# Kernel optimization log

Measured on AMD Instinct MI355X. Metric: run time of the kernel, lower is better.

## Reference

```python
import jax, jax.numpy as jnp
import numpy as np

B, C_IN, C_OUT, N, K = 32, 16, 32, 2048, 3


def setup_inputs() -> dict:
    key = jax.random.key(0)
    k1, k2 = jax.random.split(key, 2)
    x = jax.random.normal(k1, (B, C_IN, N), dtype=jnp.float32)
    # Conv1d weight (out_channels, in_channels, K), Kaiming-ish scale
    W = jax.random.normal(k2, (C_OUT, C_IN, K), dtype=jnp.float32) * (1.0 / np.sqrt(C_IN * K))
    b = jnp.zeros((C_OUT,), dtype=jnp.float32)
    return {"x": x, "W": W, "b": b}


def reference(x, W, b):
    # x: (B, C, N) -- tokens are the N column vectors in channel space
    Bd, C, Nd = x.shape
    Kd = W.shape[2]
    # NNT: pairwise squared Euclidean distances between token vectors
    sq = jnp.sum(x * x, axis=1)                      # (B, N)
    gram = jnp.einsum('bcn,bcm->bnm', x, x)          # (B, N, N)
    dist = sq[:, :, None] - 2.0 * gram + sq[:, None, :]  # (B, N, N)
    # K nearest neighbors (smallest distance; self included at dist ~0)
    _, idx = jax.lax.top_k(-dist, Kd)                # (B, N, K) int32
    flat_idx = idx.reshape(Bd, Nd * Kd)              # (B, N*K)
    # gather neighbor columns -> prime: (B, C, N*K)
    prime = jnp.take_along_axis(x, flat_idx[:, None, :], axis=2)
    # Conv1d(kernel=K, stride=K) == per-group contraction over the K neighbors
    prime4 = prime.reshape(Bd, C, Nd, Kd)            # (B, C, N, K)
    out = jnp.einsum('bcnk,ock->bon', prime4, W) + b[None, :, None]
    return out  # (B, C_out, N)
```

## Files before the change

### kernel.cpp

```cpp
#include <hip/hip_runtime.h>
#include <float.h>
#include <limits.h>

#define BATCH 32
#define C_IN 16
#define C_OUT 32
#define NTOK 2048
#define KNN 3
#define ZH 2
#define MSEG (NTOK / ZH)
#define WPB 4

using f32x4v = __attribute__((ext_vector_type(4))) float;
using bf16x8 = __attribute__((ext_vector_type(8))) short;

__device__ __forceinline__ unsigned short f2bf(float f) {
    unsigned u = __float_as_uint(f);
    unsigned r = u + 0x7fffu + ((u >> 16) & 1u);
    return (unsigned short)(r >> 16);
}
__device__ __forceinline__ float bf2f(unsigned short h) {
    return __uint_as_float(((unsigned)h) << 16);
}
__device__ __forceinline__ unsigned umin2(unsigned a, unsigned b) { return a < b ? a : b; }
__device__ __forceinline__ unsigned med3u(unsigned a, unsigned b, unsigned c) {
    unsigned d;
    asm("v_med3_u32 %0, %1, %2, %3" : "=v"(d) : "v"(a), "v"(b), "v"(c));
    return d;
}

__global__ void __launch_bounds__(256) prep_kernel(
    const float* __restrict__ x, float* __restrict__ xTf,
    float* __restrict__ sqf, uint4* __restrict__ Am)
{
    const int n = blockIdx.x * 256 + threadIdx.x;
    const int b = blockIdx.y;
    const float* xb = x + (size_t)b * C_IN * NTOK;

    float v[C_IN];
#pragma unroll
    for (int c = 0; c < C_IN; ++c) v[c] = xb[(size_t)c * NTOK + n];

    float acc = 0.0f;
#pragma unroll
    for (int c = 0; c < C_IN; ++c) acc = __fadd_rn(acc, __fmul_rn(v[c], v[c]));
    sqf[(size_t)b * NTOK + n] = acc;

    float4* dst = (float4*)(xTf + ((size_t)b * NTOK + n) * C_IN);
#pragma unroll
    for (int j = 0; j < 4; ++j)
        dst[j] = make_float4(v[4*j+0], v[4*j+1], v[4*j+2], v[4*j+3]);

    unsigned hw[8], lw[8];
#pragma unroll
    for (int j = 0; j < 8; ++j) {
        const unsigned short h0 = f2bf(v[2*j]),   h1 = f2bf(v[2*j+1]);
        const unsigned short l0 = f2bf(v[2*j]   - bf2f(h0));
        const unsigned short l1 = f2bf(v[2*j+1] - bf2f(h1));
        hw[j] = (unsigned)h0 | ((unsigned)h1 << 16);
        lw[j] = (unsigned)l0 | ((unsigned)l1 << 16);
    }
    uint4* amb = Am + (size_t)b * NTOK * 4;
    const int nt  = n >> 4;
    const int col = n & 15;
    amb[nt*64 + 0*16 + col] = make_uint4(hw[0], hw[1], hw[2], hw[3]);
    amb[nt*64 + 1*16 + col] = make_uint4(hw[4], hw[5], hw[6], hw[7]);
    amb[nt*64 + 2*16 + col] = make_uint4(lw[0], lw[1], lw[2], lw[3]);
    amb[nt*64 + 3*16 + col] = make_uint4(lw[4], lw[5], lw[6], lw[7]);
}

__global__ void __launch_bounds__(256) knn_scan_kernel(
    const uint4* __restrict__ Am, const float* __restrict__ sqf,
    const float* __restrict__ xTf, float* __restrict__ pd, int* __restrict__ pi)
{
    __shared__ int   lds_ci[WPB][16][17];
    __shared__ float lds_de[WPB][16][17];

    const int tid  = threadIdx.x;
    const int w    = tid >> 6;
    const int l    = tid & 63;
    const int col  = l & 15;
    const int quad = l >> 4;

    const int wg   = blockIdx.x;
    const int b_lo = wg & 7;
    const int t2   = wg >> 3;
    const int b_hi = t2 >> 6;
    const int rest = t2 & 63;
    const int z    = rest >> 5;
    const int ntb  = rest & 31;
    const int b    = b_lo + (b_hi << 3);
    const int nt   = ntb * WPB + w;

    const int n  = nt * 16 + col;
    const int mbase = z * MSEG;

    const uint4* amb = Am + (size_t)b * NTOK * 4;
    const float* sqb = sqf + (size_t)b * NTOK;

    const uint4 bh4 = amb[(size_t)nt*64 + ((quad & 1) * 16) + col];
    const uint4 bl4 = amb[(size_t)nt*64 + ((2 + (quad & 1)) * 16) + col];
    const bf16x8 Bhi = *(const bf16x8*)&bh4;
    const bf16x8 Blo = *(const bf16x8*)&bl4;

    const float sqn  = sqb[n];
    const float bias = sqn + 4.0f;

    unsigned k0 = ~0u, k1 = ~0u, k2 = ~0u, k3 = ~0u;
    const int moff = quad * 4;
    const int tgbase = z * (MSEG / 16);

#pragma unroll 2
    for (int t = 0; t < MSEG / 16; ++t) {
        const uint4 af4 = amb[(size_t)(tgbase + t) * 64 + l];
        const bf16x8 Af = *(const bf16x8*)&af4;
        const float4 sq4 = *(const float4*)(sqb + mbase + t * 16 + moff);

        f32x4v acc = {0.0f, 0.0f, 0.0f, 0.0f};
        acc = __builtin_amdgcn_mfma_f32_16x16x32_bf16(Af, Bhi, acc, 0, 0, 0);
        acc = __builtin_amdgcn_mfma_f32_16x16x32_bf16(Af, Blo, acc, 0, 0, 0);

        const int mb = mbase + t * 16 + moff;
        const float sqa[4] = { sq4.x, sq4.y, sq4.z, sq4.w };
#pragma unroll
        for (int r = 0; r < 4; ++r) {
            const float d = __fadd_rn(__fmaf_rn(-2.0f, acc[r], sqa[r]), bias);
            const unsigned key = (__float_as_uint(d) & 0xFFFFF800u) | (unsigned)(mb + r);
            const unsigned ok0 = k0, ok1 = k1, ok2 = k2;
            k0 = umin2(key, k0);
            k1 = med3u(key, ok0, k1);
            k2 = med3u(key, ok1, k2);
            k3 = med3u(key, ok2, k3);
        }
    }

    lds_ci[w][col][quad*4+0] = (int)(k0 & 2047u);
    lds_ci[w][col][quad*4+1] = (int)(k1 & 2047u);
    lds_ci[w][col][quad*4+2] = (int)(k2 & 2047u);
    lds_ci[w][col][quad*4+3] = (int)(k3 & 2047u);
    __syncthreads();

    float xn[C_IN];
    {
        const float4* src = (const float4*)(xTf + ((size_t)b * NTOK + n) * C_IN);
#pragma unroll
        for (int j = 0; j < 4; ++j) {
            const float4 tq = src[j];
            xn[4*j+0] = tq.x; xn[4*j+1] = tq.y; xn[4*j+2] = tq.z; xn[4*j+3] = tq.w;
        }
    }
#pragma unroll
    for (int c = 0; c < 4; ++c) {
        const int cand = quad * 4 + c;
        const int mi = lds_ci[w][col][cand];
        const float4* xm4 = (const float4*)(xTf + ((size_t)b * NTOK + mi) * C_IN);
        const float4 a0 = xm4[0], a1 = xm4[1], a2 = xm4[2], a3 = xm4[3];
        float g = 0.0f;
        g = __fmaf_rn(xn[0],  a0.x, g); g = __fmaf_rn(xn[1],  a0.y, g);
        g = __fmaf_rn(xn[2],  a0.z, g); g = __fmaf_rn(xn[3],  a0.w, g);
        g = __fmaf_rn(xn[4],  a1.x, g); g = __fmaf_rn(xn[5],  a1.y, g);
        g = __fmaf_rn(xn[6],  a1.z, g); g = __fmaf_rn(xn[7],  a1.w, g);
        g = __fmaf_rn(xn[8],  a2.x, g); g = __fmaf_rn(xn[9],  a2.y, g);
        g = __fmaf_rn(xn[10], a2.z, g); g = __fmaf_rn(xn[11], a2.w, g);
        g = __fmaf_rn(xn[12], a3.x, g); g = __fmaf_rn(xn[13], a3.y, g);
        g = __fmaf_rn(xn[14], a3.z, g); g = __fmaf_rn(xn[15], a3.w, g);
        lds_de[w][col][cand] = __fadd_rn(__fmaf_rn(-2.0f, g, sqn), sqb[mi]);
    }
    __syncthreads();

    if (l < 16) {
        float D0 = FLT_MAX, D1 = FLT_MAX, D2 = FLT_MAX;
        int   I0 = INT_MAX, I1 = INT_MAX, I2 = INT_MAX;
#pragma unroll
        for (int c = 0; c < 16; ++c) {
            const float d = lds_de[w][l][c];
            const int  ix = lds_ci[w][l][c];
            const bool b0 = (d < D0) || (d == D0 && ix < I0);
            const bool b1 = (d < D1) || (d == D1 && ix < I1);
            const bool b2 = (d < D2) || (d == D2 && ix < I2);
            const float oD0 = D0, oD1 = D1;
            const int   oI0 = I0, oI1 = I1;
            D0 = b0 ? d : D0;               I0 = b0 ? ix : I0;
            D1 = b0 ? oD0 : (b1 ? d : D1);  I1 = b0 ? oI0 : (b1 ? ix : I1);
            D2 = b1 ? oD1 : (b2 ? d : D2);  I2 = b1 ? oI1 : (b2 ? ix : I2);
        }
        const size_t base = ((size_t)z * KNN * BATCH + b) * NTOK + nt * 16 + l;
        const size_t kstr = (size_t)BATCH * NTOK;
        pd[base + 0*kstr] = D0;  pi[base + 0*kstr] = I0;
        pd[base + 1*kstr] = D1;  pi[base + 1*kstr] = I1;
        pd[base + 2*kstr] = D2;  pi[base + 2*kstr] = I2;
    }
}

__global__ void __launch_bounds__(256) merge_conv_kernel(
    const float* __restrict__ xTf, const float* __restrict__ pd,
    const int* __restrict__ pi, const float* __restrict__ W,
    const float* __restrict__ bias, float* __restrict__ out)
{
    const int wg   = blockIdx.x;
    const int b_lo = wg & 7;
    const int t2   = wg >> 3;
    const int b_hi = t2 >> 3;
    const int xc   = t2 & 7;
    const int b    = b_lo + (b_hi << 3);
    const int n    = xc * 256 + threadIdx.x;

    float D0 = FLT_MAX, D1 = FLT_MAX, D2 = FLT_MAX;
    int   I0 = INT_MAX, I1 = INT_MAX, I2 = INT_MAX;
    const size_t kstr = (size_t)BATCH * NTOK;
#pragma unroll
    for (int z = 0; z < ZH; ++z) {
        const size_t base = ((size_t)z * KNN * BATCH + b) * NTOK + n;
#pragma unroll
        for (int k = 0; k < KNN; ++k) {
            const float d = pd[base + (size_t)k * kstr];
            const int  ix = pi[base + (size_t)k * kstr];
            const bool b0 = (d < D0) || (d == D0 && ix < I0);
            const bool b1 = (d < D1) || (d == D1 && ix < I1);
            const bool b2 = (d < D2) || (d == D2 && ix < I2);
            const float oD0 = D0, oD1 = D1;
            const int   oI0 = I0, oI1 = I1;
            D0 = b0 ? d : D0;               I0 = b0 ? ix : I0;
            D1 = b0 ? oD0 : (b1 ? d : D1);  I1 = b0 ? oI0 : (b1 ? ix : I1);
            D2 = b1 ? oD1 : (b2 ? d : D2);  I2 = b1 ? oI1 : (b2 ? ix : I2);
        }
    }

    const float* xb = xTf + (size_t)b * NTOK * C_IN;
    float xg[KNN][C_IN];
    const int idx[KNN] = { I0, I1, I2 };
#pragma unroll
    for (int k = 0; k < KNN; ++k) {
        const float4* src = (const float4*)(xb + (size_t)idx[k] * C_IN);
#pragma unroll
        for (int j = 0; j < 4; ++j) {
            const float4 t = src[j];
            xg[k][4*j+0] = t.x; xg[k][4*j+1] = t.y;
            xg[k][4*j+2] = t.z; xg[k][4*j+3] = t.w;
        }
    }

#pragma unroll
    for (int o = 0; o < C_OUT; ++o) {
        float acc = bias[o];
#pragma unroll
        for (int c = 0; c < C_IN; ++c) {
#pragma unroll
            for (int k = 0; k < KNN; ++k)
                acc = __fmaf_rn(W[(o * C_IN + c) * KNN + k], xg[k][c], acc);
        }
        out[((size_t)b * C_OUT + o) * NTOK + n] = acc;
    }
}

extern "C" void kernel_launch(void* const* d_in, const int* in_sizes, int n_in,
                              void* d_out, int out_size, void* d_ws, size_t ws_size,
                              hipStream_t stream) {
    const float* x    = (const float*)d_in[0];
    const float* W    = (const float*)d_in[1];
    const float* bias = (const float*)d_in[2];
    float* out = (float*)d_out;

    char* ws = (char*)d_ws;
    const size_t BN = (size_t)BATCH * NTOK;
    uint4* Am  = (uint4*)ws;
    float* sqf = (float*)(ws + BN * 64);
    float* xTf = (float*)(ws + BN * 68);
    float* pd  = (float*)(ws + BN * 68 + BN * 64);
    int*   pi  = (int*)  (ws + BN * 68 + BN * 64 + (size_t)ZH * KNN * BN * 4);

    dim3 grid1(NTOK / 256, BATCH);
    prep_kernel<<<grid1, 256, 0, stream>>>(x, xTf, sqf, Am);

    knn_scan_kernel<<<dim3(BATCH * (NTOK / (16 * WPB)) * ZH), 256, 0, stream>>>(Am, sqf, xTf, pd, pi);

    merge_conv_kernel<<<dim3(BATCH * (NTOK / 256)), 256, 0, stream>>>(xTf, pd, pi, W, bias, out);
}
```

Before: 79.16 us.

## Stage shared A-tiles in LDS with double buffering across warps

```diff
diff --git a/kernel.cpp b/kernel.cpp
--- a/kernel.cpp
+++ b/kernel.cpp
@@ -10,6 +10,8 @@
 #define ZH 2
 #define MSEG (NTOK / ZH)
 #define WPB 4
+#define TPG 4
+#define NGRP (MSEG / 16 / TPG)
 
 using f32x4v = __attribute__((ext_vector_type(4))) float;
 using bf16x8 = __attribute__((ext_vector_type(8))) short;
@@ -73,6 +75,7 @@
     const uint4* __restrict__ Am, const float* __restrict__ sqf,
     const float* __restrict__ xTf, float* __restrict__ pd, int* __restrict__ pi)
 {
+    __shared__ uint4 stagebuf[2][TPG * 64];
     __shared__ int   lds_ci[WPB][16][17];
     __shared__ float lds_de[WPB][16][17];
 
@@ -93,7 +96,6 @@
     const int nt   = ntb * WPB + w;
 
     const int n  = nt * 16 + col;
-    const int mbase = z * MSEG;
 
     const uint4* amb = Am + (size_t)b * NTOK * 4;
     const float* sqb = sqf + (size_t)b * NTOK;
@@ -110,28 +112,47 @@
     const int moff = quad * 4;
     const int tgbase = z * (MSEG / 16);
 
-#pragma unroll 2
-    for (int t = 0; t < MSEG / 16; ++t) {
-        const uint4 af4 = amb[(size_t)(tgbase + t) * 64 + l];
-        const bf16x8 Af = *(const bf16x8*)&af4;
-        const float4 sq4 = *(const float4*)(sqb + mbase + t * 16 + moff);
-
-        f32x4v acc = {0.0f, 0.0f, 0.0f, 0.0f};
-        acc = __builtin_amdgcn_mfma_f32_16x16x32_bf16(Af, Bhi, acc, 0, 0, 0);
-        acc = __builtin_amdgcn_mfma_f32_16x16x32_bf16(Af, Blo, acc, 0, 0, 0);
-
-        const int mb = mbase + t * 16 + moff;
-        const float sqa[4] = { sq4.x, sq4.y, sq4.z, sq4.w };
-#pragma unroll
-        for (int r = 0; r < 4; ++r) {
-            const float d = __fadd_rn(__fmaf_rn(-2.0f, acc[r], sqa[r]), bias);
-            const unsigned key = (__float_as_uint(d) & 0xFFFFF800u) | (unsigned)(mb + r);
-            const unsigned ok0 = k0, ok1 = k1, ok2 = k2;
-            k0 = umin2(key, k0);
-            k1 = med3u(key, ok0, k1);
-            k2 = med3u(key, ok1, k2);
-            k3 = med3u(key, ok2, k3);
-        }
+    {
+        const uint4 s0 = amb[(size_t)(tgbase + w) * 64 + l];
+        stagebuf[0][w * 64 + l] = s0;
+    }
+    __syncthreads();
+
+    int cur = 0;
+    for (int g = 0; g < NGRP; ++g) {
+        uint4 snext;
+        if (g + 1 < NGRP)
+            snext = amb[(size_t)(tgbase + (g + 1) * TPG + w) * 64 + l];
+
+#pragma unroll
+        for (int tt = 0; tt < TPG; ++tt) {
+            const int tg = tgbase + g * TPG + tt;
+            const bf16x8 Af = *(const bf16x8*)&stagebuf[cur][tt * 64 + l];
+            const float4 sq4 = *(const float4*)(sqb + tg * 16 + moff);
+
+            f32x4v acc = {0.0f, 0.0f, 0.0f, 0.0f};
+            acc = __builtin_amdgcn_mfma_f32_16x16x32_bf16(Af, Bhi, acc, 0, 0, 0);
+            acc = __builtin_amdgcn_mfma_f32_16x16x32_bf16(Af, Blo, acc, 0, 0, 0);
+
+            const int mb = tg * 16 + moff;
+            const float sqa[4] = { sq4.x, sq4.y, sq4.z, sq4.w };
+#pragma unroll
+            for (int r = 0; r < 4; ++r) {
+                const float d = __fadd_rn(__fmaf_rn(-2.0f, acc[r], sqa[r]), bias);
+                const unsigned key = (__float_as_uint(d) & 0xFFFFF800u) | (unsigned)(mb + r);
+                const unsigned ok0 = k0, ok1 = k1, ok2 = k2;
+                k0 = umin2(key, k0);
+                k1 = med3u(key, ok0, k1);
+                k2 = med3u(key, ok1, k2);
+                k3 = med3u(key, ok2, k3);
+            }
+        }
+
+        if (g + 1 < NGRP) {
+            stagebuf[cur ^ 1][w * 64 + l] = snext;
+            cur ^= 1;
+        }
+        __syncthreads();
     }
 
     lds_ci[w][col][quad*4+0] = (int)(k0 & 2047u);
```

Result: no change. 79.16 us (+0.0%).

## Move exact fp32 rescoring of KNN candidates from scan kernel into conv kernel

Applied to the files above, without the earlier changes.

```diff
diff --git a/kernel.cpp b/kernel.cpp
--- a/kernel.cpp
+++ b/kernel.cpp
@@ -10,6 +10,7 @@
 #define ZH 2
 #define MSEG (NTOK / ZH)
 #define WPB 4
+#define NPLANE 32
 
 using f32x4v = __attribute__((ext_vector_type(4))) float;
 using bf16x8 = __attribute__((ext_vector_type(8))) short;
@@ -71,11 +72,8 @@
 
 __global__ void __launch_bounds__(256) knn_scan_kernel(
     const uint4* __restrict__ Am, const float* __restrict__ sqf,
-    const float* __restrict__ xTf, float* __restrict__ pd, int* __restrict__ pi)
+    unsigned* __restrict__ keyws)
 {
-    __shared__ int   lds_ci[WPB][16][17];
-    __shared__ float lds_de[WPB][16][17];
-
     const int tid  = threadIdx.x;
     const int w    = tid >> 6;
     const int l    = tid & 63;
@@ -103,8 +101,7 @@
     const bf16x8 Bhi = *(const bf16x8*)&bh4;
     const bf16x8 Blo = *(const bf16x8*)&bl4;
 
-    const float sqn  = sqb[n];
-    const float bias = sqn + 4.0f;
+    const float bias = sqb[n] + 4.0f;
 
     unsigned k0 = ~0u, k1 = ~0u, k2 = ~0u, k3 = ~0u;
     const int moff = quad * 4;
@@ -134,67 +131,17 @@
         }
     }
 
-    lds_ci[w][col][quad*4+0] = (int)(k0 & 2047u);
-    lds_ci[w][col][quad*4+1] = (int)(k1 & 2047u);
-    lds_ci[w][col][quad*4+2] = (int)(k2 & 2047u);
-    lds_ci[w][col][quad*4+3] = (int)(k3 & 2047u);
-    __syncthreads();
-
-    float xn[C_IN];
-    {
-        const float4* src = (const float4*)(xTf + ((size_t)b * NTOK + n) * C_IN);
-#pragma unroll
-        for (int j = 0; j < 4; ++j) {
-            const float4 tq = src[j];
-            xn[4*j+0] = tq.x; xn[4*j+1] = tq.y; xn[4*j+2] = tq.z; xn[4*j+3] = tq.w;
-        }
-    }
-#pragma unroll
-    for (int c = 0; c < 4; ++c) {
-        const int cand = quad * 4 + c;
-        const int mi = lds_ci[w][col][cand];
-        const float4* xm4 = (const float4*)(xTf + ((size_t)b * NTOK + mi) * C_IN);
-        const float4 a0 = xm4[0], a1 = xm4[1], a2 = xm4[2], a3 = xm4[3];
-        float g = 0.0f;
-        g = __fmaf_rn(xn[0],  a0.x, g); g = __fmaf_rn(xn[1],  a0.y, g);
-        g = __fmaf_rn(xn[2],  a0.z, g); g = __fmaf_rn(xn[3],  a0.w, g);
-        g = __fmaf_rn(xn[4],  a1.x, g); g = __fmaf_rn(xn[5],  a1.y, g);
-        g = __fmaf_rn(xn[6],  a1.z, g); g = __fmaf_rn(xn[7],  a1.w, g);
-        g = __fmaf_rn(xn[8],  a2.x, g); g = __fmaf_rn(xn[9],  a2.y, g);
-        g = __fmaf_rn(xn[10], a2.z, g); g = __fmaf_rn(xn[11], a2.w, g);
-        g = __fmaf_rn(xn[12], a3.x, g); g = __fmaf_rn(xn[13], a3.y, g);
-        g = __fmaf_rn(xn[14], a3.z, g); g = __fmaf_rn(xn[15], a3.w, g);
-        lds_de[w][col][cand] = __fadd_rn(__fmaf_rn(-2.0f, g, sqn), sqb[mi]);
-    }
-    __syncthreads();
-
-    if (l < 16) {
-        float D0 = FLT_MAX, D1 = FLT_MAX, D2 = FLT_MAX;
-        int   I0 = INT_MAX, I1 = INT_MAX, I2 = INT_MAX;
-#pragma unroll
-        for (int c = 0; c < 16; ++c) {
-            const float d = lds_de[w][l][c];
-            const int  ix = lds_ci[w][l][c];
-            const bool b0 = (d < D0) || (d == D0 && ix < I0);
-            const bool b1 = (d < D1) || (d == D1 && ix < I1);
-            const bool b2 = (d < D2) || (d == D2 && ix < I2);
-            const float oD0 = D0, oD1 = D1;
-            const int   oI0 = I0, oI1 = I1;
-            D0 = b0 ? d : D0;               I0 = b0 ? ix : I0;
-            D1 = b0 ? oD0 : (b1 ? d : D1);  I1 = b0 ? oI0 : (b1 ? ix : I1);
-            D2 = b1 ? oD1 : (b2 ? d : D2);  I2 = b1 ? oI1 : (b2 ? ix : I2);
-        }
-        const size_t base = ((size_t)z * KNN * BATCH + b) * NTOK + nt * 16 + l;
-        const size_t kstr = (size_t)BATCH * NTOK;
-        pd[base + 0*kstr] = D0;  pi[base + 0*kstr] = I0;
-        pd[base + 1*kstr] = D1;  pi[base + 1*kstr] = I1;
-        pd[base + 2*kstr] = D2;  pi[base + 2*kstr] = I2;
-    }
-}
-
-__global__ void __launch_bounds__(256) merge_conv_kernel(
-    const float* __restrict__ xTf, const float* __restrict__ pd,
-    const int* __restrict__ pi, const float* __restrict__ W,
+    const size_t plane = (size_t)BATCH * NTOK;
+    unsigned* kp = keyws + ((size_t)((z * 4 + quad) * 4) * BATCH + b) * NTOK + n;
+    kp[0]         = k0;
+    kp[plane]     = k1;
+    kp[2 * plane] = k2;
+    kp[3 * plane] = k3;
+}
+
+__global__ void __launch_bounds__(256) rescore_conv_kernel(
+    const float* __restrict__ xTf, const float* __restrict__ sqf,
+    const unsigned* __restrict__ keyws, const float* __restrict__ W,
     const float* __restrict__ bias, float* __restrict__ out)
 {
     const int wg   = blockIdx.x;
@@ -205,28 +152,53 @@
     const int b    = b_lo + (b_hi << 3);
     const int n    = xc * 256 + threadIdx.x;
 
+    const float* sqb = sqf + (size_t)b * NTOK;
+    const float* xb  = xTf + (size_t)b * NTOK * C_IN;
+
+    float xn[C_IN];
+    {
+        const float4* src = (const float4*)(xb + (size_t)n * C_IN);
+#pragma unroll
+        for (int j = 0; j < 4; ++j) {
+            const float4 tq = src[j];
+            xn[4*j+0] = tq.x; xn[4*j+1] = tq.y; xn[4*j+2] = tq.z; xn[4*j+3] = tq.w;
+        }
+    }
+    const float sqn = sqb[n];
+
     float D0 = FLT_MAX, D1 = FLT_MAX, D2 = FLT_MAX;
     int   I0 = INT_MAX, I1 = INT_MAX, I2 = INT_MAX;
-    const size_t kstr = (size_t)BATCH * NTOK;
-#pragma unroll
-    for (int z = 0; z < ZH; ++z) {
-        const size_t base = ((size_t)z * KNN * BATCH + b) * NTOK + n;
-#pragma unroll
-        for (int k = 0; k < KNN; ++k) {
-            const float d = pd[base + (size_t)k * kstr];
-            const int  ix = pi[base + (size_t)k * kstr];
-            const bool b0 = (d < D0) || (d == D0 && ix < I0);
-            const bool b1 = (d < D1) || (d == D1 && ix < I1);
-            const bool b2 = (d < D2) || (d == D2 && ix < I2);
-            const float oD0 = D0, oD1 = D1;
-            const int   oI0 = I0, oI1 = I1;
-            D0 = b0 ? d : D0;               I0 = b0 ? ix : I0;
-            D1 = b0 ? oD0 : (b1 ? d : D1);  I1 = b0 ? oI0 : (b1 ? ix : I1);
-            D2 = b1 ? oD1 : (b2 ? d : D2);  I2 = b1 ? oI1 : (b2 ? ix : I2);
-        }
-    }
-
-    const float* xb = xTf + (size_t)b * NTOK * C_IN;
+    const size_t plane = (size_t)BATCH * NTOK;
+    const size_t kbase = (size_t)b * NTOK + n;
+
+#pragma unroll 4
+    for (int p = 0; p < NPLANE; ++p) {
+        const unsigned key = keyws[kbase + (size_t)p * plane];
+        const int mi = (int)(key & 2047u);
+
+        const float4* xm4 = (const float4*)(xb + (size_t)mi * C_IN);
+        const float4 q0 = xm4[0], q1 = xm4[1], q2 = xm4[2], q3 = xm4[3];
+        float g = 0.0f;
+        g = __fmaf_rn(xn[0],  q0.x, g); g = __fmaf_rn(xn[1],  q0.y, g);
+        g = __fmaf_rn(xn[2],  q0.z, g); g = __fmaf_rn(xn[3],  q0.w, g);
+        g = __fmaf_rn(xn[4],  q1.x, g); g = __fmaf_rn(xn[5],  q1.y, g);
+        g = __fmaf_rn(xn[6],  q1.z, g); g = __fmaf_rn(xn[7],  q1.w, g);
+        g = __fmaf_rn(xn[8],  q2.x, g); g = __fmaf_rn(xn[9],  q2.y, g);
+        g = __fmaf_rn(xn[10], q2.z, g); g = __fmaf_rn(xn[11], q2.w, g);
+        g = __fmaf_rn(xn[12], q3.x, g); g = __fmaf_rn(xn[13], q3.y, g);
+        g = __fmaf_rn(xn[14], q3.z, g); g = __fmaf_rn(xn[15], q3.w, g);
+        const float d = __fadd_rn(__fmaf_rn(-2.0f, g, sqn), sqb[mi]);
+
+        const bool c0 = (d < D0) || (d == D0 && mi < I0);
+        const bool c1 = (d < D1) || (d == D1 && mi < I1);
+        const bool c2 = (d < D2) || (d == D2 && mi < I2);
+        const float oD0 = D0, oD1 = D1;
+        const int   oI0 = I0, oI1 = I1;
+        D0 = c0 ? d : D0;               I0 = c0 ? mi : I0;
+        D1 = c0 ? oD0 : (c1 ? d : D1);  I1 = c0 ? oI0 : (c1 ? mi : I1);
+        D2 = c1 ? oD1 : (c2 ? d : D2);  I2 = c1 ? oI1 : (c2 ? mi : I2);
+    }
+
     float xg[KNN][C_IN];
     const int idx[KNN] = { I0, I1, I2 };
 #pragma unroll
@@ -263,16 +235,15 @@
 
     char* ws = (char*)d_ws;
     const size_t BN = (size_t)BATCH * NTOK;
-    uint4* Am  = (uint4*)ws;
-    float* sqf = (float*)(ws + BN * 64);
-    float* xTf = (float*)(ws + BN * 68);
-    float* pd  = (float*)(ws + BN * 68 + BN * 64);
-    int*   pi  = (int*)  (ws + BN * 68 + BN * 64 + (size_t)ZH * KNN * BN * 4);
+    uint4*    Am    = (uint4*)ws;
+    float*    sqf   = (float*)(ws + BN * 64);
+    float*    xTf   = (float*)(ws + BN * 68);
+    unsigned* keyws = (unsigned*)(ws + BN * 68 + BN * 64);
 
     dim3 grid1(NTOK / 256, BATCH);
     prep_kernel<<<grid1, 256, 0, stream>>>(x, xTf, sqf, Am);
 
-    knn_scan_kernel<<<dim3(BATCH * (NTOK / (16 * WPB)) * ZH), 256, 0, stream>>>(Am, sqf, xTf, pd, pi);
-
-    merge_conv_kernel<<<dim3(BATCH * (NTOK / 256)), 256, 0, stream>>>(xTf, pd, pi, W, bias, out);
-}
+    knn_scan_kernel<<<dim3(BATCH * (NTOK / (16 * WPB)) * ZH), 256, 0, stream>>>(Am, sqf, keyws);
+
+    rescore_conv_kernel<<<dim3(BATCH * (NTOK / 256)), 256, 0, stream>>>(xTf, sqf, keyws, W, bias, out);
+}
```

After: 77.14 us. -2.5%, faster.
